# Performance work log

Measured on AMD Instinct MI355X. Metric: run time of the kernel, lower is better.

Reference implementation:

```python
import jax, jax.numpy as jnp
import numpy as np

K = 16  # matches init kwarg k


def setup_inputs() -> dict:
    key = jax.random.key(0)
    point_cloud = jax.random.normal(key, (4, 64, 4096), dtype=jnp.float32)
    return {"point_cloud": point_cloud}


def reference(point_cloud):
    B, dims, N = point_cloud.shape
    xt = jnp.transpose(point_cloud, (0, 2, 1))  # (B, N, dims)
    # pairwise euclidean distances (cdist, p=2)
    sq = jnp.sum(xt * xt, axis=-1)  # (B, N)
    d2 = sq[:, :, None] + sq[:, None, :] - 2.0 * jnp.einsum('bnd,bmd->bnm', xt, xt)
    dist = jnp.sqrt(jnp.maximum(d2, 0.0))  # (B, N, N)
    # k+1 smallest distances; drop self (first) neighbor
    _, idx_o = jax.lax.top_k(-dist, K + 1)  # (B, N, K+1)
    idx = idx_o[:, :, 1:]  # (B, N, K)
    # gather neighbor features: neighbors[b,d,n,j] = point_cloud[b,d,idx[b,n,j]]
    neighbors = jax.vmap(lambda pc, i: pc[:, i])(point_cloud, idx)  # (B, dims, N, K)
    central = point_cloud[:, :, :, None]  # (B, dims, N, 1)
    edge_feature = jnp.concatenate(
        [jnp.broadcast_to(central, (B, dims, N, K)), neighbors - central], axis=1
    )  # (B, 2*dims, N, K)
    return edge_feature, idx.reshape(B, -1)
```

## Files before the change

### kernel.cpp

```cpp
#include <hip/hip_runtime.h>


#define BATCH 4
#define DIMS 64
#define NPTS 4096
#define KNN 16
#define NCHUNK 32
#define CHLEN 128
#define GSZ 8
#define RN (BATCH * NPTS)
#define MLANES 8
#define MCH (NCHUNK / MLANES)

typedef unsigned long long u64;
typedef unsigned int u32;

__device__ __forceinline__ double sentinel() {
    return __longlong_as_double(0x7FEFFFFFFFFFFFFFLL);
}

__global__ __launch_bounds__(256) void ef_sq_kernel(const float* __restrict__ pc,
                                                    float* __restrict__ sq) {
    int gid = blockIdx.x * 256 + threadIdx.x;
    int b = gid >> 12;
    int n = gid & (NPTS - 1);
    const float* p = pc + (size_t)b * DIMS * NPTS + n;
    float r[8];
#pragma unroll
    for (int j = 0; j < 8; ++j) {
        float v = p[(size_t)j * NPTS];
        r[j] = __fmul_rn(v, v);
    }
#pragma unroll
    for (int i = 8; i < DIMS; i += 8) {
#pragma unroll
        for (int j = 0; j < 8; ++j) {
            float v = p[(size_t)(i + j) * NPTS];
            r[j] = __fadd_rn(r[j], __fmul_rn(v, v));
        }
    }
    float t01 = __fadd_rn(r[0], r[1]);
    float t23 = __fadd_rn(r[2], r[3]);
    float t45 = __fadd_rn(r[4], r[5]);
    float t67 = __fadd_rn(r[6], r[7]);
    sq[gid] = __fadd_rn(__fadd_rn(t01, t23), __fadd_rn(t45, t67));
}

__global__ __launch_bounds__(256, 3) void ef_knn_partial(const float* __restrict__ pc,
                                                         const float* __restrict__ sq,
                                                         u64* __restrict__ pKey) {
    __shared__ float tile[DIMS][CHLEN];
    __shared__ float tileSq[CHLEN];
    int tid = threadIdx.x;
    int r = blockIdx.x * 256 + tid;
    int c = blockIdx.y;
    int b = (blockIdx.x * 256) >> 12;
    int n = r & (NPTS - 1);
    int m0 = c * CHLEN;
    const float* pcb = pc + (size_t)b * DIMS * NPTS;

    float xr[DIMS];
#pragma unroll
    for (int d = 0; d < DIMS; ++d) xr[d] = pcb[(size_t)d * NPTS + n];
#pragma unroll
    for (int d = 0; d < DIMS; ++d) asm volatile("" : "+v"(xr[d]));
    float sqn = sq[r];

#pragma unroll
    for (int i = 0; i < 8; ++i) {
        int idx = tid + i * 256;
        int d = idx >> 5;
        int mq = idx & 31;
        float4 v = *(const float4*)(pcb + (size_t)d * NPTS + m0 + mq * 4);
        *(float4*)&tile[d][mq * 4] = v;
    }
    if (tid < CHLEN / 4)
        *(float4*)&tileSq[tid * 4] =
            *(const float4*)(sq + (size_t)b * NPTS + m0 + tid * 4);
    __syncthreads();

    double key[KNN];
#pragma unroll
    for (int j = 0; j < KNN; ++j) key[j] = sentinel();

    for (int g = 0; g < CHLEN; g += GSZ) {
        float acc[GSZ];
#pragma unroll
        for (int j = 0; j < GSZ; ++j) acc[j] = 0.f;
#pragma unroll
        for (int d = 0; d < DIMS; ++d) {
            float xv = xr[d];
            float4 lo = *(const float4*)&tile[d][g];
            float4 hi = *(const float4*)&tile[d][g + 4];
            acc[0] = fmaf(xv, lo.x, acc[0]);
            acc[1] = fmaf(xv, lo.y, acc[1]);
            acc[2] = fmaf(xv, lo.z, acc[2]);
            acc[3] = fmaf(xv, lo.w, acc[3]);
            acc[4] = fmaf(xv, hi.x, acc[4]);
            acc[5] = fmaf(xv, hi.y, acc[5]);
            acc[6] = fmaf(xv, hi.z, acc[6]);
            acc[7] = fmaf(xv, hi.w, acc[7]);
        }
        float4 sq_lo = *(const float4*)&tileSq[g];
        float4 sq_hi = *(const float4*)&tileSq[g + 4];
        float sqv[GSZ] = {sq_lo.x, sq_lo.y, sq_lo.z, sq_lo.w,
                          sq_hi.x, sq_hi.y, sq_hi.z, sq_hi.w};
        double s[GSZ];
#pragma unroll
        for (int j = 0; j < GSZ; ++j) {
            int m = m0 + g + j;
            float t1 = __fadd_rn(sqn, sqv[j]);
            float d2 = __fsub_rn(t1, __fmul_rn(2.0f, acc[j]));
            float dist = __fsqrt_rn(fmaxf(d2, 0.f));
            u64 cu = ((u64)__float_as_uint(dist) << 32) | (u64)(u32)m;
            double cand = __longlong_as_double((long long)cu);
            s[j] = (m == n) ? sentinel() : cand;
        }
#define CE8(i, jj) { double lo_ = fmin(s[i], s[jj]); double hi_ = fmax(s[i], s[jj]); s[i] = lo_; s[jj] = hi_; }
        CE8(0, 1) CE8(2, 3) CE8(4, 5) CE8(6, 7)
        CE8(0, 2) CE8(1, 3) CE8(4, 6) CE8(5, 7)
        CE8(1, 2) CE8(5, 6)
        CE8(0, 4) CE8(1, 5) CE8(2, 6) CE8(3, 7)
        CE8(2, 4) CE8(3, 5)
        CE8(1, 2) CE8(3, 4) CE8(5, 6)
#undef CE8
#pragma unroll
        for (int j = 8; j < 16; ++j) key[j] = fmin(key[j], s[15 - j]);
#pragma unroll
        for (int st = 8; st >= 1; st >>= 1) {
#pragma unroll
            for (int j = 0; j < KNN; ++j) {
                if ((j & st) == 0) {
                    double a = key[j], d = key[j | st];
                    key[j] = fmin(a, d);
                    key[j | st] = fmax(a, d);
                }
            }
        }
    }

    u64* dst = pKey + ((size_t)c * RN + r) * KNN;
#pragma unroll
    for (int j = 0; j < KNN; ++j) dst[j] = (u64)__double_as_longlong(key[j]);
}

__global__ __launch_bounds__(256) void ef_knn_merge(const u64* __restrict__ pKey,
                                                    float* __restrict__ outIdxF) {
    int t = blockIdx.x * 256 + threadIdx.x;
    int r = t >> 3;
    int s = t & 7;
    double key[KNN];
    {
        const u64* src = pKey + ((size_t)(s * MCH) * RN + r) * KNN;
#pragma unroll
        for (int j = 0; j < KNN; ++j)
            key[j] = __longlong_as_double((long long)src[j]);
    }
    for (int ci = 1; ci < MCH; ++ci) {
        const u64* src = pKey + ((size_t)(s * MCH + ci) * RN + r) * KNN;
        double v[KNN];
#pragma unroll
        for (int j = 0; j < KNN; ++j)
            v[j] = __longlong_as_double((long long)src[j]);
#pragma unroll
        for (int j = 0; j < KNN; ++j) key[j] = fmin(key[j], v[KNN - 1 - j]);
#pragma unroll
        for (int st = 8; st >= 1; st >>= 1) {
#pragma unroll
            for (int j = 0; j < KNN; ++j) {
                if ((j & st) == 0) {
                    double a = key[j], d = key[j | st];
                    key[j] = fmin(a, d);
                    key[j | st] = fmax(a, d);
                }
            }
        }
    }
#pragma unroll
    for (int mask = 1; mask <= 4; mask <<= 1) {
        double oth[KNN];
#pragma unroll
        for (int j = 0; j < KNN; ++j) oth[j] = __shfl_xor(key[j], mask, 64);
#pragma unroll
        for (int j = 0; j < KNN; ++j) key[j] = fmin(key[j], oth[KNN - 1 - j]);
#pragma unroll
        for (int st = 8; st >= 1; st >>= 1) {
#pragma unroll
            for (int j = 0; j < KNN; ++j) {
                if ((j & st) == 0) {
                    double a = key[j], d = key[j | st];
                    key[j] = fmin(a, d);
                    key[j | st] = fmax(a, d);
                }
            }
        }
    }
    if (s == 0) {
        float* dstf = outIdxF + (size_t)r * KNN;
#pragma unroll
        for (int j = 0; j < KNN; ++j)
            dstf[j] = (float)(u32)((u64)__double_as_longlong(key[j]) & 0xFFFFFFFFu);
    }
}

__global__ __launch_bounds__(256) void ef_edge_kernel(const float* __restrict__ pc,
                                                      const float* __restrict__ idxF,
                                                      float* __restrict__ out) {
    int gid = blockIdx.x * 256 + threadIdx.x;
    int b = gid >> 16;
    int nk = gid & 65535;
    int n = nk >> 4;
    int m = (int)idxF[gid];
    const float* pcb = pc + (size_t)b * DIMS * NPTS;
    float* ob = out + (size_t)b * 2 * DIMS * NPTS * KNN;
#pragma unroll
    for (int d = 0; d < DIMS; ++d) {
        float cv = pcb[(size_t)d * NPTS + n];
        float nv = pcb[(size_t)d * NPTS + m];
        ob[(size_t)d * (NPTS * KNN) + nk] = cv;
        ob[(size_t)(DIMS + d) * (NPTS * KNN) + nk] = nv - cv;
    }
}

extern "C" void kernel_launch(void* const* d_in, const int* in_sizes, int n_in,
                              void* d_out, int out_size, void* d_ws, size_t ws_size,
                              hipStream_t stream) {
    const float* pc = (const float*)d_in[0];
    float* out = (float*)d_out;

    u64* pKey = (u64*)d_out;
    float* sq = out + 16777216;
    float* outIdxF = out + (size_t)BATCH * 2 * DIMS * NPTS * KNN;

    ef_sq_kernel<<<(BATCH * NPTS) / 256, 256, 0, stream>>>(pc, sq);
    ef_knn_partial<<<dim3((BATCH * NPTS) / 256, NCHUNK), 256, 0, stream>>>(pc, sq, pKey);
    ef_knn_merge<<<(BATCH * NPTS * MLANES) / 256, 256, 0, stream>>>(pKey, outIdxF);
    ef_edge_kernel<<<(BATCH * NPTS * KNN) / 256, 256, 0, stream>>>(pc, outIdxF, out);
}
```

Before: 336.3 us.

## Widen KNN candidate groups to 16 and gather edges from transposed point cloud

The partial KNN kernel now processes 16 candidates per group, using two 8-sorters plus a bitonic merge before merging into the running top-16. This roughly halves the number of costly 16-wide merge networks per chunk but raises register pressure. Separately, a transpose kernel writes a point-major copy into the workspace so the edge kernel can gather neighbor rows with float4 loads and write four k-values per thread with vector stores. The transposed path runs only when the workspace is large enough.

```diff
diff --git a/kernel.cpp b/kernel.cpp
--- a/kernel.cpp
+++ b/kernel.cpp
@@ -7,7 +7,7 @@
 #define KNN 16
 #define NCHUNK 32
 #define CHLEN 128
-#define GSZ 8
+#define GSZ 16
 #define RN (BATCH * NPTS)
 #define MLANES 8
 #define MCH (NCHUNK / MLANES)
@@ -44,6 +44,30 @@
     float t45 = __fadd_rn(r[4], r[5]);
     float t67 = __fadd_rn(r[6], r[7]);
     sq[gid] = __fadd_rn(__fadd_rn(t01, t23), __fadd_rn(t45, t67));
+}
+
+__global__ __launch_bounds__(256) void ef_transpose(const float* __restrict__ pc,
+                                                    float* __restrict__ pcT) {
+    __shared__ float smT[DIMS][65];
+    int tid = threadIdx.x;
+    int m0 = blockIdx.x * 64;
+    int b = blockIdx.y;
+    const float* pcb = pc + (size_t)b * DIMS * NPTS;
+#pragma unroll
+    for (int i = 0; i < 16; ++i) {
+        int idx = i * 256 + tid;
+        int d = idx >> 6;
+        int m = idx & 63;
+        smT[d][m] = pcb[(size_t)d * NPTS + m0 + m];
+    }
+    __syncthreads();
+#pragma unroll
+    for (int i = 0; i < 16; ++i) {
+        int idx = i * 256 + tid;
+        int m = idx >> 6;
+        int d = idx & 63;
+        pcT[((size_t)b * NPTS + m0 + m) * DIMS + d] = smT[d][m];
+    }
 }
 
 __global__ __launch_bounds__(256, 3) void ef_knn_partial(const float* __restrict__ pc,
@@ -83,6 +107,8 @@
 #pragma unroll
     for (int j = 0; j < KNN; ++j) key[j] = sentinel();
 
+#define CE(arr, i, jj) { double lo_ = fmin(arr[i], arr[jj]); double hi_ = fmax(arr[i], arr[jj]); arr[i] = lo_; arr[jj] = hi_; }
+
     for (int g = 0; g < CHLEN; g += GSZ) {
         float acc[GSZ];
 #pragma unroll
@@ -90,21 +116,33 @@
 #pragma unroll
         for (int d = 0; d < DIMS; ++d) {
             float xv = xr[d];
-            float4 lo = *(const float4*)&tile[d][g];
-            float4 hi = *(const float4*)&tile[d][g + 4];
-            acc[0] = fmaf(xv, lo.x, acc[0]);
-            acc[1] = fmaf(xv, lo.y, acc[1]);
-            acc[2] = fmaf(xv, lo.z, acc[2]);
-            acc[3] = fmaf(xv, lo.w, acc[3]);
-            acc[4] = fmaf(xv, hi.x, acc[4]);
-            acc[5] = fmaf(xv, hi.y, acc[5]);
-            acc[6] = fmaf(xv, hi.z, acc[6]);
-            acc[7] = fmaf(xv, hi.w, acc[7]);
-        }
-        float4 sq_lo = *(const float4*)&tileSq[g];
-        float4 sq_hi = *(const float4*)&tileSq[g + 4];
-        float sqv[GSZ] = {sq_lo.x, sq_lo.y, sq_lo.z, sq_lo.w,
-                          sq_hi.x, sq_hi.y, sq_hi.z, sq_hi.w};
+            float4 q0 = *(const float4*)&tile[d][g];
+            float4 q1 = *(const float4*)&tile[d][g + 4];
+            float4 q2 = *(const float4*)&tile[d][g + 8];
+            float4 q3 = *(const float4*)&tile[d][g + 12];
+            acc[0]  = fmaf(xv, q0.x, acc[0]);
+            acc[1]  = fmaf(xv, q0.y, acc[1]);
+            acc[2]  = fmaf(xv, q0.z, acc[2]);
+            acc[3]  = fmaf(xv, q0.w, acc[3]);
+            acc[4]  = fmaf(xv, q1.x, acc[4]);
+            acc[5]  = fmaf(xv, q1.y, acc[5]);
+            acc[6]  = fmaf(xv, q1.z, acc[6]);
+            acc[7]  = fmaf(xv, q1.w, acc[7]);
+            acc[8]  = fmaf(xv, q2.x, acc[8]);
+            acc[9]  = fmaf(xv, q2.y, acc[9]);
+            acc[10] = fmaf(xv, q2.z, acc[10]);
+            acc[11] = fmaf(xv, q2.w, acc[11]);
+            acc[12] = fmaf(xv, q3.x, acc[12]);
+            acc[13] = fmaf(xv, q3.y, acc[13]);
+            acc[14] = fmaf(xv, q3.z, acc[14]);
+            acc[15] = fmaf(xv, q3.w, acc[15]);
+        }
+        float4 s0 = *(const float4*)&tileSq[g];
+        float4 s1 = *(const float4*)&tileSq[g + 4];
+        float4 s2 = *(const float4*)&tileSq[g + 8];
+        float4 s3 = *(const float4*)&tileSq[g + 12];
+        float sqv[GSZ] = {s0.x, s0.y, s0.z, s0.w, s1.x, s1.y, s1.z, s1.w,
+                          s2.x, s2.y, s2.z, s2.w, s3.x, s3.y, s3.z, s3.w};
         double s[GSZ];
 #pragma unroll
         for (int j = 0; j < GSZ; ++j) {
@@ -116,16 +154,31 @@
             double cand = __longlong_as_double((long long)cu);
             s[j] = (m == n) ? sentinel() : cand;
         }
-#define CE8(i, jj) { double lo_ = fmin(s[i], s[jj]); double hi_ = fmax(s[i], s[jj]); s[i] = lo_; s[jj] = hi_; }
-        CE8(0, 1) CE8(2, 3) CE8(4, 5) CE8(6, 7)
-        CE8(0, 2) CE8(1, 3) CE8(4, 6) CE8(5, 7)
-        CE8(1, 2) CE8(5, 6)
-        CE8(0, 4) CE8(1, 5) CE8(2, 6) CE8(3, 7)
-        CE8(2, 4) CE8(3, 5)
-        CE8(1, 2) CE8(3, 4) CE8(5, 6)
-#undef CE8
-#pragma unroll
-        for (int j = 8; j < 16; ++j) key[j] = fmin(key[j], s[15 - j]);
+        CE(s, 0, 1) CE(s, 2, 3) CE(s, 4, 5) CE(s, 6, 7)
+        CE(s, 0, 2) CE(s, 1, 3) CE(s, 4, 6) CE(s, 5, 7)
+        CE(s, 1, 2) CE(s, 5, 6)
+        CE(s, 0, 4) CE(s, 1, 5) CE(s, 2, 6) CE(s, 3, 7)
+        CE(s, 2, 4) CE(s, 3, 5)
+        CE(s, 1, 2) CE(s, 3, 4) CE(s, 5, 6)
+
+        CE(s, 8, 9) CE(s, 10, 11) CE(s, 12, 13) CE(s, 14, 15)
+        CE(s, 8, 10) CE(s, 9, 11) CE(s, 12, 14) CE(s, 13, 15)
+        CE(s, 9, 10) CE(s, 13, 14)
+        CE(s, 8, 12) CE(s, 9, 13) CE(s, 10, 14) CE(s, 11, 15)
+        CE(s, 10, 12) CE(s, 11, 13)
+        CE(s, 9, 10) CE(s, 11, 12) CE(s, 13, 14)
+
+        CE(s, 0, 15) CE(s, 1, 14) CE(s, 2, 13) CE(s, 3, 12)
+        CE(s, 4, 11) CE(s, 5, 10) CE(s, 6, 9)  CE(s, 7, 8)
+        CE(s, 0, 4)  CE(s, 1, 5)  CE(s, 2, 6)  CE(s, 3, 7)
+        CE(s, 8, 12) CE(s, 9, 13) CE(s, 10, 14) CE(s, 11, 15)
+        CE(s, 0, 2)  CE(s, 1, 3)  CE(s, 4, 6)  CE(s, 5, 7)
+        CE(s, 8, 10) CE(s, 9, 11) CE(s, 12, 14) CE(s, 13, 15)
+        CE(s, 0, 1)  CE(s, 2, 3)  CE(s, 4, 5)  CE(s, 6, 7)
+        CE(s, 8, 9)  CE(s, 10, 11) CE(s, 12, 13) CE(s, 14, 15)
+
+#pragma unroll
+        for (int j = 0; j < KNN; ++j) key[j] = fmin(key[j], s[KNN - 1 - j]);
 #pragma unroll
         for (int st = 8; st >= 1; st >>= 1) {
 #pragma unroll
@@ -138,6 +191,7 @@
             }
         }
     }
+#undef CE
 
     u64* dst = pKey + ((size_t)c * RN + r) * KNN;
 #pragma unroll
@@ -200,6 +254,51 @@
 #pragma unroll
         for (int j = 0; j < KNN; ++j)
             dstf[j] = (float)(u32)((u64)__double_as_longlong(key[j]) & 0xFFFFFFFFu);
+    }
+}
+
+__global__ __launch_bounds__(256) void ef_edge_kernelT(const float* __restrict__ pcT,
+                                                       const float* __restrict__ idxF,
+                                                       float* __restrict__ out) {
+    int t = blockIdx.x * 256 + threadIdx.x;
+    int b = t >> 14;
+    int rem = t & 16383;
+    int n = rem >> 2;
+    int k0 = (rem & 3) * 4;
+    float4 i4 = *(const float4*)(idxF + (((size_t)(b << 12) + n) << 4) + k0);
+    int m0 = (int)i4.x, m1 = (int)i4.y, m2 = (int)i4.z, m3 = (int)i4.w;
+    const float4* cr  = (const float4*)(pcT + ((size_t)(b << 12) + n)  * DIMS);
+    const float4* nr0 = (const float4*)(pcT + ((size_t)(b << 12) + m0) * DIMS);
+    const float4* nr1 = (const float4*)(pcT + ((size_t)(b << 12) + m1) * DIMS);
+    const float4* nr2 = (const float4*)(pcT + ((size_t)(b << 12) + m2) * DIMS);
+    const float4* nr3 = (const float4*)(pcT + ((size_t)(b << 12) + m3) * DIMS);
+    float* ob = out + (size_t)b * 2 * DIMS * NPTS * KNN + (size_t)n * KNN + k0;
+#pragma unroll
+    for (int q = 0; q < DIMS / 4; ++q) {
+        float4 c4 = cr[q];
+        float4 a0 = nr0[q], a1 = nr1[q], a2 = nr2[q], a3 = nr3[q];
+        float cv, nv0, nv1, nv2, nv3;
+        float4 st;
+        cv = c4.x; nv0 = a0.x; nv1 = a1.x; nv2 = a2.x; nv3 = a3.x;
+        st = make_float4(cv, cv, cv, cv);
+        *(float4*)(ob + (size_t)(4 * q + 0) * (NPTS * KNN)) = st;
+        st = make_float4(nv0 - cv, nv1 - cv, nv2 - cv, nv3 - cv);
+        *(float4*)(ob + (size_t)(DIMS + 4 * q + 0) * (NPTS * KNN)) = st;
+        cv = c4.y; nv0 = a0.y; nv1 = a1.y; nv2 = a2.y; nv3 = a3.y;
+        st = make_float4(cv, cv, cv, cv);
+        *(float4*)(ob + (size_t)(4 * q + 1) * (NPTS * KNN)) = st;
+        st = make_float4(nv0 - cv, nv1 - cv, nv2 - cv, nv3 - cv);
+        *(float4*)(ob + (size_t)(DIMS + 4 * q + 1) * (NPTS * KNN)) = st;
+        cv = c4.z; nv0 = a0.z; nv1 = a1.z; nv2 = a2.z; nv3 = a3.z;
+        st = make_float4(cv, cv, cv, cv);
+        *(float4*)(ob + (size_t)(4 * q + 2) * (NPTS * KNN)) = st;
+        st = make_float4(nv0 - cv, nv1 - cv, nv2 - cv, nv3 - cv);
+        *(float4*)(ob + (size_t)(DIMS + 4 * q + 2) * (NPTS * KNN)) = st;
+        cv = c4.w; nv0 = a0.w; nv1 = a1.w; nv2 = a2.w; nv3 = a3.w;
+        st = make_float4(cv, cv, cv, cv);
+        *(float4*)(ob + (size_t)(4 * q + 3) * (NPTS * KNN)) = st;
+        st = make_float4(nv0 - cv, nv1 - cv, nv2 - cv, nv3 - cv);
+        *(float4*)(ob + (size_t)(DIMS + 4 * q + 3) * (NPTS * KNN)) = st;
     }
 }
 
@@ -231,9 +330,16 @@
     u64* pKey = (u64*)d_out;
     float* sq = out + 16777216;
     float* outIdxF = out + (size_t)BATCH * 2 * DIMS * NPTS * KNN;
+    float* pcT = (float*)d_ws;
+    bool useT = ws_size >= (size_t)BATCH * NPTS * DIMS * sizeof(float);
 
     ef_sq_kernel<<<(BATCH * NPTS) / 256, 256, 0, stream>>>(pc, sq);
+    if (useT)
+        ef_transpose<<<dim3(NPTS / 64, BATCH), 256, 0, stream>>>(pc, pcT);
     ef_knn_partial<<<dim3((BATCH * NPTS) / 256, NCHUNK), 256, 0, stream>>>(pc, sq, pKey);
     ef_knn_merge<<<(BATCH * NPTS * MLANES) / 256, 256, 0, stream>>>(pKey, outIdxF);
-    ef_edge_kernel<<<(BATCH * NPTS * KNN) / 256, 256, 0, stream>>>(pc, outIdxF, out);
-}
+    if (useT)
+        ef_edge_kernelT<<<(BATCH * NPTS * KNN / 4) / 256, 256, 0, stream>>>(pcT, outIdxF, out);
+    else
+        ef_edge_kernel<<<(BATCH * NPTS * KNN) / 256, 256, 0, stream>>>(pc, outIdxF, out);
+}
```

Measured after the change: 325.1 us. 3.3% less time.
